# Kernel optimization log

Hardware: AMD Instinct MI355X
Metric: run time of the kernel (lower is better)

Reference implementation:

```python
import jax, jax.numpy as jnp
import numpy as np

EMB_DIM = 128
HIDDEN = 1024
CL_TEMPERATURE = 0.5
NUM_LABELS = 20
EPS = 1e-14


def setup_inputs() -> dict:
    key = jax.random.key(0)
    k1, k2, k3, k4, k5, k6 = jax.random.split(key, 6)
    B, L = 4, 128
    token_repr = jax.random.normal(k1, (B, L, HIDDEN), dtype=jnp.float32)
    labels = jax.random.randint(k2, (B, L), 0, NUM_LABELS, dtype=jnp.int64)
    mask = jnp.ones((B, L), dtype=jnp.int64)
    # Linear params (PyTorch default init scale ~ U(-1/sqrt(fan_in), 1/sqrt(fan_in)))
    s = 1.0 / np.sqrt(HIDDEN)
    W_mu = jax.random.uniform(k3, (HIDDEN, EMB_DIM), jnp.float32, -s, s)
    b_mu = jax.random.uniform(k4, (EMB_DIM,), jnp.float32, -s, s)
    W_sigma = jax.random.uniform(k5, (HIDDEN, EMB_DIM), jnp.float32, -s, s)
    b_sigma = jax.random.uniform(k6, (EMB_DIM,), jnp.float32, -s, s)
    return {"token_repr": token_repr, "labels": labels, "mask": mask,
            "W_mu": W_mu, "b_mu": b_mu, "W_sigma": W_sigma, "b_sigma": b_sigma}


def _pairwise_sym_kl(mu, sigma):
    """Symmetric diagonal-Gaussian KL between all pairs. mu,sigma: [N,D] -> [N,N]."""
    D = mu.shape[-1]
    mu_i, mu_j = mu[:, None, :], mu[None, :, :]          # [N,N,D] broadcast
    si, sj = sigma[:, None, :], sigma[None, :, :]
    r_ij = sj / si                                        # [N,N,D]
    ij_kl = 0.5 * (r_ij.sum(-1)
                   + (((mu_i - mu_j) ** 2) / si).sum(-1)
                   - D
                   - jnp.log(r_ij + EPS).sum(-1))
    r_ji = si / sj
    ji_kl = 0.5 * (r_ji.sum(-1)
                   + (((mu_j - mu_i) ** 2) / sj).sum(-1)
                   - D
                   - jnp.log(r_ji + EPS).sum(-1))
    return 0.5 * (ij_kl + ji_kl)


def reference(token_repr, labels, mask, W_mu, b_mu, W_sigma, b_sigma):
    h = jax.nn.relu(token_repr)                           # nn.ReLU before Linear
    mu = (h @ W_mu + b_mu).reshape(-1, EMB_DIM)           # [N,D]
    sigma = (jax.nn.elu(h @ W_sigma + b_sigma) + 1.0 + EPS).reshape(-1, EMB_DIM)
    lab = labels.reshape(-1)
    valid = (mask.reshape(-1) == 1) & (lab > 0)           # torch does this by filtering; we mask

    # loss = -symmetric KL for all pairs (cl_type='kl')
    loss = -_pairwise_sym_kl(mu, sigma)                   # [N,N]

    # denominator mask: all embedding dims differ (excludes self / duplicates)
    all_diff = jnp.all(mu[:, None, :] != mu[None, :, :], axis=-1)
    den_mask = all_diff & valid[:, None] & valid[None, :]
    num_mask = den_mask & (lab[:, None] == lab[None, :])

    # NT-Xent with masked reduction; rows with zero positives (or invalid) dropped
    e = jnp.exp(loss / CL_TEMPERATURE)                    # kl >= 0 so e <= 1, stable
    cnts = jnp.sum(num_mask, axis=1).astype(loss.dtype)
    loss_num = jnp.sum(e * num_mask, axis=1)
    loss_den = jnp.sum(e * den_mask, axis=1)
    include = cnts > 0
    safe = lambda x: jnp.where(include, x, 1.0)
    loss_final = -jnp.log(safe(loss_num)) + jnp.log(safe(loss_den)) + jnp.log(safe(cnts))
    n_inc = jnp.maximum(jnp.sum(include), 1).astype(loss.dtype)
    return jnp.sum(jnp.where(include, loss_final, 0.0)) / n_inc
```

## Files before the change

### kernel.cpp

```cpp
#include <hip/hip_runtime.h>
#include <math.h>

#define N_TOK 512
#define DIM   128
#define KDIM  1024
#define EPSF  1e-14f

__global__ __launch_bounds__(512) void projT(
    const float* __restrict__ token, const float* __restrict__ Wmu,
    const float* __restrict__ bmu, const float* __restrict__ Wsg,
    const float* __restrict__ bsg, float* __restrict__ mu,
    float* __restrict__ sg, float* __restrict__ iv,
    float* __restrict__ jmuT, float2* __restrict__ jsviT)
{
    __shared__ float hs[8][KDIM];
    __shared__ float4 red[7][8][8];
    const int bid = blockIdx.x;
    const int t = threadIdx.x;

    const int rowg = bid >> 3, sel = bid & 7;
    const int m = sel >> 2, ch = sel & 3;

    {
        const float4* src = (const float4*)(token + (size_t)rowg * 8 * KDIM);
        float4* dst = (float4*)&hs[0][0];
        #pragma unroll
        for (int r = 0; r < 4; ++r) {
            int idx = t + r * 512;
            float4 v = src[idx];
            v.x = fmaxf(v.x, 0.f); v.y = fmaxf(v.y, 0.f);
            v.z = fmaxf(v.z, 0.f); v.w = fmaxf(v.w, 0.f);
            dst[idx] = v;
        }
    }
    __syncthreads();

    const int q = t & 7, rsub = t >> 3;
    const int row = rsub & 7, kq = rsub >> 3;
    const int d = ch * 32 + q * 4;
    const float* __restrict__ W = (m ? Wsg : Wmu) + (size_t)(kq * 128) * DIM + d;
    const float4* hp = (const float4*)(&hs[row][kq * 128]);

    float4 acc = make_float4(0.f, 0.f, 0.f, 0.f);
    #pragma unroll 4
    for (int k4 = 0; k4 < 32; ++k4) {
        float4 h = hp[k4];
        const float* wp = W + (size_t)(k4 * 4) * DIM;
        float4 w0 = *(const float4*)(wp);
        float4 w1 = *(const float4*)(wp + DIM);
        float4 w2 = *(const float4*)(wp + 2 * DIM);
        float4 w3 = *(const float4*)(wp + 3 * DIM);
        acc.x = fmaf(h.x, w0.x, acc.x); acc.y = fmaf(h.x, w0.y, acc.y);
        acc.z = fmaf(h.x, w0.z, acc.z); acc.w = fmaf(h.x, w0.w, acc.w);
        acc.x = fmaf(h.y, w1.x, acc.x); acc.y = fmaf(h.y, w1.y, acc.y);
        acc.z = fmaf(h.y, w1.z, acc.z); acc.w = fmaf(h.y, w1.w, acc.w);
        acc.x = fmaf(h.z, w2.x, acc.x); acc.y = fmaf(h.z, w2.y, acc.y);
        acc.z = fmaf(h.z, w2.z, acc.z); acc.w = fmaf(h.z, w2.w, acc.w);
        acc.x = fmaf(h.w, w3.x, acc.x); acc.y = fmaf(h.w, w3.y, acc.y);
        acc.z = fmaf(h.w, w3.z, acc.z); acc.w = fmaf(h.w, w3.w, acc.w);
    }

    if (kq > 0) red[kq - 1][row][q] = acc;
    __syncthreads();
    if (kq == 0) {
        #pragma unroll
        for (int s = 0; s < 7; ++s) {
            float4 r = red[s][row][q];
            acc.x += r.x; acc.y += r.y; acc.z += r.z; acc.w += r.w;
        }
        const int rowi = rowg * 8 + row;
        if (m == 0) {
            float4 b = *(const float4*)(bmu + d);
            acc.x += b.x; acc.y += b.y; acc.z += b.z; acc.w += b.w;
            *(float4*)(mu + (size_t)rowi * DIM + d) = acc;
            jmuT[(size_t)(d + 0) * N_TOK + rowi] = acc.x;
            jmuT[(size_t)(d + 1) * N_TOK + rowi] = acc.y;
            jmuT[(size_t)(d + 2) * N_TOK + rowi] = acc.z;
            jmuT[(size_t)(d + 3) * N_TOK + rowi] = acc.w;
        } else {
            float4 b = *(const float4*)(bsg + d);
            float x0 = acc.x + b.x, x1 = acc.y + b.y;
            float x2 = acc.z + b.z, x3 = acc.w + b.w;
            float4 e, vv;
            e.x = (x0 > 0.f ? x0 : expm1f(x0)) + 1.0f + EPSF;
            e.y = (x1 > 0.f ? x1 : expm1f(x1)) + 1.0f + EPSF;
            e.z = (x2 > 0.f ? x2 : expm1f(x2)) + 1.0f + EPSF;
            e.w = (x3 > 0.f ? x3 : expm1f(x3)) + 1.0f + EPSF;
            vv.x = 1.0f / e.x; vv.y = 1.0f / e.y;
            vv.z = 1.0f / e.z; vv.w = 1.0f / e.w;
            *(float4*)(sg + (size_t)rowi * DIM + d) = e;
            *(float4*)(iv + (size_t)rowi * DIM + d) = vv;
            jsviT[(size_t)(d + 0) * N_TOK + rowi] = make_float2(e.x, vv.x);
            jsviT[(size_t)(d + 1) * N_TOK + rowi] = make_float2(e.y, vv.y);
            jsviT[(size_t)(d + 2) * N_TOK + rowi] = make_float2(e.z, vv.z);
            jsviT[(size_t)(d + 3) * N_TOK + rowi] = make_float2(e.w, vv.w);
        }
    }
}

__global__ __launch_bounds__(512) void pair_kernel(
    const float* __restrict__ mu, const float* __restrict__ sg,
    const float* __restrict__ iv, const float* __restrict__ jmuT,
    const float2* __restrict__ jsviT, const int* __restrict__ labels,
    const int* __restrict__ mask, float* __restrict__ gpart)
{
    __shared__ float si[3][16][DIM];
    __shared__ int slab[16], svalid[16];
    const int ig = blockIdx.x >> 4, jg = blockIdx.x & 15;
    const int i0 = ig * 16, j0 = jg * 32;
    const int t = threadIdx.x;

    {
        int row = t >> 5, kq = t & 31;
        size_t off = (size_t)(i0 + row) * DIM + kq * 4;
        ((float4*)&si[0][0][0])[t] = *(const float4*)(mu + off);
        ((float4*)&si[1][0][0])[t] = *(const float4*)(sg + off);
        ((float4*)&si[2][0][0])[t] = *(const float4*)(iv + off);
    }
    if (t < 16) {
        int lab = labels[i0 + t];
        slab[t] = lab;
        svalid[t] = (mask[i0 + t] == 1 && lab > 0) ? 1 : 0;
    }
    __syncthreads();

    const int jl = t & 31, il = t >> 5;
    const int j = j0 + jl;
    const int labj = labels[j];
    const bool validj = (mask[j] == 1) && (labj > 0);

    const float*  pmT = jmuT  + j;
    const float2* psT = jsviT + j;

    float acc = 0.f;
    float mn = 1e30f;

    #pragma unroll 4
    for (int q = 0; q < 32; ++q) {
        const int d0 = q * 4;
        float  jm0 = pmT[(size_t)(d0 + 0) * N_TOK];
        float  jm1 = pmT[(size_t)(d0 + 1) * N_TOK];
        float  jm2 = pmT[(size_t)(d0 + 2) * N_TOK];
        float  jm3 = pmT[(size_t)(d0 + 3) * N_TOK];
        float2 sv0 = psT[(size_t)(d0 + 0) * N_TOK];
        float2 sv1 = psT[(size_t)(d0 + 1) * N_TOK];
        float2 sv2 = psT[(size_t)(d0 + 2) * N_TOK];
        float2 sv3 = psT[(size_t)(d0 + 3) * N_TOK];

        float4 bm = *(const float4*)(&si[0][il][d0]);
        float4 bs = *(const float4*)(&si[1][il][d0]);
        float4 bv = *(const float4*)(&si[2][il][d0]);

        float dm;
        dm = bm.x - jm0; acc = fmaf(fmaf(dm, dm, sv0.x), bv.x, fmaf(fmaf(dm, dm, bs.x), sv0.y, acc)); mn = fminf(mn, fabsf(dm));
        dm = bm.y - jm1; acc = fmaf(fmaf(dm, dm, sv1.x), bv.y, fmaf(fmaf(dm, dm, bs.y), sv1.y, acc)); mn = fminf(mn, fabsf(dm));
        dm = bm.z - jm2; acc = fmaf(fmaf(dm, dm, sv2.x), bv.z, fmaf(fmaf(dm, dm, bs.z), sv2.y, acc)); mn = fminf(mn, fabsf(dm));
        dm = bm.w - jm3; acc = fmaf(fmaf(dm, dm, sv3.x), bv.w, fmaf(fmaf(dm, dm, bs.w), sv3.y, acc)); mn = fminf(mn, fabsf(dm));
    }

    float e = expf(128.0f - 0.5f * acc);
    bool pv = validj && (svalid[il] != 0) && (mn != 0.0f);
    bool sm = pv && (labj == slab[il]);
    float dd = pv ? e : 0.f, nn = sm ? e : 0.f, cc = sm ? 1.f : 0.f;

    #pragma unroll
    for (int m = 1; m < 32; m <<= 1) {
        cc += __shfl_xor(cc, m); nn += __shfl_xor(nn, m); dd += __shfl_xor(dd, m);
    }
    if (jl == 0) {
        float* pa = gpart + ((size_t)jg * N_TOK + i0 + il) * 3;
        pa[0] = cc; pa[1] = nn; pa[2] = dd;
    }
}

__global__ __launch_bounds__(512) void final_kernel(
    const float* __restrict__ gpart, float* __restrict__ out)
{
    __shared__ float redL[8], redI[8];
    const int t = threadIdx.x;
    float c = 0.f, nm = 0.f, dn = 0.f;
    #pragma unroll
    for (int jg = 0; jg < 16; ++jg) {
        const float* p = gpart + ((size_t)jg * N_TOK + t) * 3;
        c += p[0]; nm += p[1]; dn += p[2];
    }
    const bool inc = c > 0.5f;
    float lf = inc ? (-logf(nm) + logf(dn) + logf(c)) : 0.f;
    float fi = inc ? 1.f : 0.f;
    #pragma unroll
    for (int m = 1; m < 64; m <<= 1) {
        lf += __shfl_xor(lf, m);
        fi += __shfl_xor(fi, m);
    }
    if ((t & 63) == 0) { redL[t >> 6] = lf; redI[t >> 6] = fi; }
    __syncthreads();
    if (t == 0) {
        float L = 0.f, I = 0.f;
        #pragma unroll
        for (int w = 0; w < 8; ++w) { L += redL[w]; I += redI[w]; }
        out[0] = L / fmaxf(I, 1.0f);
    }
}

extern "C" void kernel_launch(void* const* d_in, const int* in_sizes, int n_in,
                              void* d_out, int out_size, void* d_ws, size_t ws_size,
                              hipStream_t stream) {
    const float* token  = (const float*)d_in[0];
    const int*   labels = (const int*)d_in[1];
    const int*   mask   = (const int*)d_in[2];
    const float* Wmu    = (const float*)d_in[3];
    const float* bmu    = (const float*)d_in[4];
    const float* Wsg    = (const float*)d_in[5];
    const float* bsg    = (const float*)d_in[6];

    float*  ws    = (float*)d_ws;
    float*  mu    = ws;
    float*  sg    = mu + 65536;
    float*  iv    = sg + 65536;
    float*  jmuT  = iv + 65536;
    float2* jsviT = (float2*)(jmuT + 65536);
    float*  gpart = (float*)(jsviT + 65536);

    projT<<<512, 512, 0, stream>>>(token, Wmu, bmu, Wsg, bsg, mu, sg, iv,
                                   jmuT, jsviT);
    pair_kernel<<<512, 512, 0, stream>>>(mu, sg, iv, jmuT, jsviT, labels, mask,
                                         gpart);
    final_kernel<<<1, 512, 0, stream>>>(gpart, (float*)d_out);
}
```

Measured before the change: 109.6 us.

## Exploit symmetry of pairwise KL to compute only upper-triangular tiles

The pair kernel now launches one block per upper-triangular 16x16 tile (528 blocks of 256 threads) instead of covering the full 512x512 matrix. Each off-diagonal tile's results are reduced along both rows and columns, so it writes partials for rows i and for rows j, and the final kernel sums 32 partial groups per row. This roughly halves the pairwise KL work, which is the dominant cost. In exchange it adds a triangular index decode, an extra shared-memory column reduction with a barrier, and more partial sums for the final kernel to read.

```diff
diff --git a/kernel.cpp b/kernel.cpp
--- a/kernel.cpp
+++ b/kernel.cpp
@@ -98,24 +98,36 @@
     }
 }
 
-__global__ __launch_bounds__(512) void pair_kernel(
+__global__ __launch_bounds__(256) void pair_sym(
     const float* __restrict__ mu, const float* __restrict__ sg,
     const float* __restrict__ iv, const float* __restrict__ jmuT,
     const float2* __restrict__ jsviT, const int* __restrict__ labels,
     const int* __restrict__ mask, float* __restrict__ gpart)
 {
     __shared__ float si[3][16][DIM];
+    __shared__ float mred[4][16][3];
     __shared__ int slab[16], svalid[16];
-    const int ig = blockIdx.x >> 4, jg = blockIdx.x & 15;
-    const int i0 = ig * 16, j0 = jg * 32;
     const int t = threadIdx.x;
 
+    const int k = blockIdx.x;
+    int R = (int)((65.0f - sqrtf(4225.0f - 8.0f * (float)k)) * 0.5f);
+    R = R < 0 ? 0 : (R > 31 ? 31 : R);
+    while (R > 0 && (32 * R - R * (R - 1) / 2) > k) --R;
+    while (R < 31 && (32 * (R + 1) - (R + 1) * R / 2) <= k) ++R;
+    const int C = R + (k - (32 * R - R * (R - 1) / 2));
+    const int i0 = R * 16, j0 = C * 16;
+    const bool diag = (R == C);
+
     {
-        int row = t >> 5, kq = t & 31;
-        size_t off = (size_t)(i0 + row) * DIM + kq * 4;
-        ((float4*)&si[0][0][0])[t] = *(const float4*)(mu + off);
-        ((float4*)&si[1][0][0])[t] = *(const float4*)(sg + off);
-        ((float4*)&si[2][0][0])[t] = *(const float4*)(iv + off);
+        #pragma unroll
+        for (int rep = 0; rep < 2; ++rep) {
+            int f = t + rep * 256;
+            int row = f >> 5, kq = f & 31;
+            size_t off = (size_t)(i0 + row) * DIM + kq * 4;
+            ((float4*)&si[0][0][0])[f] = *(const float4*)(mu + off);
+            ((float4*)&si[1][0][0])[f] = *(const float4*)(sg + off);
+            ((float4*)&si[2][0][0])[f] = *(const float4*)(iv + off);
+        }
     }
     if (t < 16) {
         int lab = labels[i0 + t];
@@ -124,7 +136,7 @@
     }
     __syncthreads();
 
-    const int jl = t & 31, il = t >> 5;
+    const int jl = t & 15, il = t >> 4;
     const int j = j0 + jl;
     const int labj = labels[j];
     const bool validj = (mask[j] == 1) && (labj > 0);
@@ -163,13 +175,32 @@
     bool sm = pv && (labj == slab[il]);
     float dd = pv ? e : 0.f, nn = sm ? e : 0.f, cc = sm ? 1.f : 0.f;
 
+    float ic = cc, in = nn, id = dd;
     #pragma unroll
-    for (int m = 1; m < 32; m <<= 1) {
-        cc += __shfl_xor(cc, m); nn += __shfl_xor(nn, m); dd += __shfl_xor(dd, m);
+    for (int m = 1; m < 16; m <<= 1) {
+        ic += __shfl_xor(ic, m); in += __shfl_xor(in, m); id += __shfl_xor(id, m);
     }
     if (jl == 0) {
-        float* pa = gpart + ((size_t)jg * N_TOK + i0 + il) * 3;
-        pa[0] = cc; pa[1] = nn; pa[2] = dd;
+        float* pa = gpart + ((size_t)C * N_TOK + i0 + il) * 3;
+        pa[0] = ic; pa[1] = in; pa[2] = id;
+    }
+
+    if (!diag) {
+        float mc = cc, mm = nn, md = dd;
+        mc += __shfl_xor(mc, 16); mm += __shfl_xor(mm, 16); md += __shfl_xor(md, 16);
+        mc += __shfl_xor(mc, 32); mm += __shfl_xor(mm, 32); md += __shfl_xor(md, 32);
+        const int w = t >> 6;
+        if ((t & 63) < 16) {
+            mred[w][jl][0] = mc; mred[w][jl][1] = mm; mred[w][jl][2] = md;
+        }
+        __syncthreads();
+        if (t < 16) {
+            float c4 = mred[0][t][0] + mred[1][t][0] + mred[2][t][0] + mred[3][t][0];
+            float n4 = mred[0][t][1] + mred[1][t][1] + mred[2][t][1] + mred[3][t][1];
+            float d4 = mred[0][t][2] + mred[1][t][2] + mred[2][t][2] + mred[3][t][2];
+            float* pb = gpart + ((size_t)R * N_TOK + j0 + t) * 3;
+            pb[0] = c4; pb[1] = n4; pb[2] = d4;
+        }
     }
 }
 
@@ -180,8 +211,8 @@
     const int t = threadIdx.x;
     float c = 0.f, nm = 0.f, dn = 0.f;
     #pragma unroll
-    for (int jg = 0; jg < 16; ++jg) {
-        const float* p = gpart + ((size_t)jg * N_TOK + t) * 3;
+    for (int g = 0; g < 32; ++g) {
+        const float* p = gpart + ((size_t)g * N_TOK + t) * 3;
         c += p[0]; nm += p[1]; dn += p[2];
     }
     const bool inc = c > 0.5f;
@@ -223,7 +254,7 @@
 
     projT<<<512, 512, 0, stream>>>(token, Wmu, bmu, Wsg, bsg, mu, sg, iv,
                                    jmuT, jsviT);
-    pair_kernel<<<512, 512, 0, stream>>>(mu, sg, iv, jmuT, jsviT, labels, mask,
-                                         gpart);
+    pair_sym<<<528, 256, 0, stream>>>(mu, sg, iv, jmuT, jsviT, labels, mask,
+                                      gpart);
     final_kernel<<<1, 512, 0, stream>>>(gpart, (float*)d_out);
 }
```

New measurement: 108.7 us. No clear change (-0.8%).
